# Kernel optimization log

Measured on AMD Instinct MI355X. Metric: run time of the kernel, lower is better.

## Reference

```python
import jax, jax.numpy as jnp
import numpy as np

D_HEAD = 128
WINDOW = 512
SCALE = D_HEAD ** -0.5

def setup_inputs() -> dict:
    key = jax.random.key(0)
    kq, kk, kv = jax.random.split(key, 3)
    shape = (4, 16, 2048, D_HEAD)  # [B, H, T, d_head]
    q = jax.random.normal(kq, shape, dtype=jnp.float32)
    k = jax.random.normal(kk, shape, dtype=jnp.float32)
    v = jax.random.normal(kv, shape, dtype=jnp.float32)
    return {"q": q, "k": k, "v": v}

def reference(q, k, v):
    # Sliding-window causal attention (BaseAttention._sliding_window_attention).
    T = q.shape[2]
    scores = jnp.einsum('bhqd,bhkd->bhqk', q, k) * SCALE  # [B,H,T,T]
    i = jnp.arange(T)
    causal = i[None, :] <= i[:, None]                      # j <= i
    in_window = (i[:, None] - i[None, :]) < WINDOW         # i - j < window
    mask = causal & in_window
    scores = jnp.where(mask, scores, -jnp.inf)
    attn = jax.nn.softmax(scores.astype(jnp.float32), axis=-1).astype(v.dtype)
    return jnp.einsum('bhqk,bhkd->bhqd', attn, v)
```

## Files before the change

kernel.cpp:

```cpp
#include <hip/hip_runtime.h>

#define T_SEQ   2048
#define DH      128
#define WINDOW  512
#define BM      128
#define BN      64
#define NT      32
#define TILE_US 16384
#define SCALE_LOG2E 0.12751744250f

typedef unsigned short ushort_t;
typedef __attribute__((ext_vector_type(8))) unsigned short ushort8;
typedef __attribute__((ext_vector_type(4))) unsigned short ushort4v;
typedef __attribute__((ext_vector_type(4))) float float4v;
typedef __attribute__((ext_vector_type(16))) float float16v;
typedef __attribute__((ext_vector_type(8))) __bf16 bf16x8;

union U8 { ushort8 us; bf16x8 bf; unsigned u[4]; };
union FU { float f; unsigned u; };

__device__ __forceinline__ unsigned short f2bf(float f) {
  FU x; x.f = f;
  unsigned r = x.u + 0x7FFFu + ((x.u >> 16) & 1u);
  return (unsigned short)(r >> 16);
}

__device__ __forceinline__ void async16(const ushort_t* g, ushort_t* l) {
  __builtin_amdgcn_global_load_lds(
      (const __attribute__((address_space(1))) unsigned int*)g,
      (__attribute__((address_space(3))) unsigned int*)l, 16, 0, 0);
}

__global__ __launch_bounds__(256)
void pack_kv(const float* __restrict__ kg, const float* __restrict__ vg,
             ushort_t* __restrict__ ws)
{
  __shared__ __align__(16) ushort_t sb[TILE_US];
  const int tile = blockIdx.x;
  const int tid  = threadIdx.x;
  const size_t src = (size_t)tile * (BN * DH);
  const float* kb = kg + src;
  const float* vb = vg + src;

#pragma unroll
  for (int rep = 0; rep < 4; ++rep) {
    const int b   = rep * 256 + tid;
    const int key = b >> 4;
    const int c8  = b & 15;
    const float* s = kb + key * DH + c8 * 8;
    float4v a = *(const float4v*)s;
    float4v c = *(const float4v*)(s + 4);
    U8 h;
    h.us[0]=f2bf(a[0]); h.us[1]=f2bf(a[1]); h.us[2]=f2bf(a[2]); h.us[3]=f2bf(a[3]);
    h.us[4]=f2bf(c[0]); h.us[5]=f2bf(c[1]); h.us[6]=f2bf(c[2]); h.us[7]=f2bf(c[3]);
    *(ushort8*)(sb + key * DH + ((c8 ^ (key & 7)) << 3)) = h.us;
  }

  {
    const int cb  = tid >> 3;
    const int rb0 = tid & 7;
#pragma unroll
    for (int it = 0; it < 2; ++it) {
      const int rb = rb0 + it * 8;
      const float* s = vb + (size_t)(rb * 4) * DH + cb * 4;
      float4v r0 = *(const float4v*)(s);
      float4v r1 = *(const float4v*)(s + DH);
      float4v r2 = *(const float4v*)(s + 2 * DH);
      float4v r3 = *(const float4v*)(s + 3 * DH);
      const int B    = (rb & 1) | ((rb >> 2) << 1);
      const int off4 = ((rb >> 1) & 1) << 2;
#pragma unroll
      for (int c = 0; c < 4; ++c) {
        const int d = cb * 4 + c;
        ushort4v h;
        h[0]=f2bf(r0[c]); h[1]=f2bf(r1[c]); h[2]=f2bf(r2[c]); h[3]=f2bf(r3[c]);
        *(ushort4v*)(sb + 8192 + d * BN + ((B ^ (d & 7)) << 3) + off4) = h;
      }
    }
  }
  __syncthreads();

  ushort_t* wt = ws + (size_t)tile * TILE_US;
#pragma unroll
  for (int rep = 0; rep < 8; ++rep) {
    const int off = (rep * 256 + tid) * 8;
    *(ushort8*)(wt + off) = *(const ushort8*)(sb + off);
  }
}

__global__ __launch_bounds__(256, 3)
void swa_fwd(const float* __restrict__ qg, const ushort_t* __restrict__ ws,
             float* __restrict__ og)
{
  __shared__ __align__(16) ushort_t lds[TILE_US];

  const int qt   = (gridDim.x - 1) - blockIdx.x;
  const int bh   = blockIdx.y;
  const int tid  = threadIdx.x;
  const int wv   = tid >> 6;
  const int lane = tid & 63;
  const int l32  = lane & 31;
  const int half = lane >> 5;
  const int l7   = l32 & 7;

  const size_t base = (size_t)bh * (T_SEQ * DH);
  const float* qb = qg + base;
  float*       ob = og + base;
  const ushort_t* wsb = ws + (size_t)bh * NT * TILE_US;

  const int i0w = qt * BM + wv * 32;
  const int iq  = i0w + l32;

  bf16x8 qf[8];
  {
    const float* qrow = qb + (size_t)iq * DH + half * 8;
#pragma unroll
    for (int ks = 0; ks < 8; ++ks) {
      float4v a = *(const float4v*)(qrow + ks * 16);
      float4v b = *(const float4v*)(qrow + ks * 16 + 4);
      U8 u;
      u.us[0]=f2bf(a[0]*SCALE_LOG2E); u.us[1]=f2bf(a[1]*SCALE_LOG2E);
      u.us[2]=f2bf(a[2]*SCALE_LOG2E); u.us[3]=f2bf(a[3]*SCALE_LOG2E);
      u.us[4]=f2bf(b[0]*SCALE_LOG2E); u.us[5]=f2bf(b[1]*SCALE_LOG2E);
      u.us[6]=f2bf(b[2]*SCALE_LOG2E); u.us[7]=f2bf(b[3]*SCALE_LOG2E);
      qf[ks] = u.bf;
    }
  }

  float16v O[4];
#pragma unroll
  for (int dc = 0; dc < 4; ++dc) O[dc] = (float16v)(0.0f);
  float m = -1e30f, l = 0.f;

  const int lo  = qt * BM - (WINDOW - 1);
  const int kt0 = (lo > 0) ? (lo >> 6) : 0;
  const int kt1 = 2 * qt + 1;

  for (int kt = kt0; kt <= kt1; ++kt) {
    {
      const ushort_t* wt = wsb + (size_t)kt * TILE_US;
#pragma unroll
      for (int rd = 0; rd < 8; ++rd) {
        const int off = (rd * 256 + tid) * 8;
        async16(wt + off, lds + off);
      }
    }
    __syncthreads();

    const int j0 = kt * BN;
    const bool active = (j0 <= i0w + 31) && (i0w - j0 - 63 < WINDOW);
    if (active) {
      float16v sv[2];
#pragma unroll
      for (int c = 0; c < 2; ++c) {
        float16v acc = (float16v)(0.0f);
        const ushort_t* krow = lds + (c * 32 + l32) * DH;
#pragma unroll
        for (int ks = 0; ks < 8; ++ks) {
          U8 a; a.us = *(const ushort8*)(krow + (((2 * ks + half) ^ l7) << 3));
          acc = __builtin_amdgcn_mfma_f32_32x32x16_bf16(a.bf, qf[ks], acc, 0, 0, 0);
        }
        sv[c] = acc;
      }

      const bool full = (j0 + 63 <= i0w) && ((i0w + 31) - j0 < WINDOW);
      if (!full) {
#pragma unroll
        for (int c = 0; c < 2; ++c) {
#pragma unroll
          for (int r = 0; r < 16; ++r) {
            const int j = j0 + c * 32 + (r & 3) + 8 * (r >> 2) + 4 * half;
            const bool ok = (j <= iq) && ((iq - j) < WINDOW);
            sv[c][r] = ok ? sv[c][r] : -1e30f;
          }
        }
      }

      float mt = sv[0][0];
#pragma unroll
      for (int r = 1; r < 16; ++r) mt = fmaxf(mt, sv[0][r]);
#pragma unroll
      for (int r = 0; r < 16; ++r) mt = fmaxf(mt, sv[1][r]);
      mt = fmaxf(mt, __shfl_xor(mt, 32));
      const float mn = fmaxf(m, mt);
      const float alpha = __builtin_amdgcn_exp2f(m - mn);
      m = mn;

      float ps = 0.f;
      unsigned pk[2][8];
#pragma unroll
      for (int c = 0; c < 2; ++c) {
#pragma unroll
        for (int rg = 0; rg < 8; ++rg) {
          FU p0, p1;
          p0.f = __builtin_amdgcn_exp2f(sv[c][2 * rg]     - m);
          p1.f = __builtin_amdgcn_exp2f(sv[c][2 * rg + 1] - m);
          p0.u &= 0xFFFF0000u; p1.u &= 0xFFFF0000u;
          ps += p0.f + p1.f;
          pk[c][rg] = (p0.u >> 16) | p1.u;
        }
      }
      l = l * alpha + ps;
#pragma unroll
      for (int dc = 0; dc < 4; ++dc)
#pragma unroll
        for (int r = 0; r < 16; ++r) O[dc][r] *= alpha;

#pragma unroll
      for (int s = 0; s < 4; ++s) {
        const int c = s >> 1, o = (s & 1) * 4;
        U8 b;
        b.u[0] = pk[c][o]; b.u[1] = pk[c][o + 1];
        b.u[2] = pk[c][o + 2]; b.u[3] = pk[c][o + 3];
        const int blk = ((2 * s + half) ^ l7) << 3;
#pragma unroll
        for (int dc = 0; dc < 4; ++dc) {
          U8 a; a.us = *(const ushort8*)(lds + 8192 + (dc * 32 + l32) * BN + blk);
          O[dc] = __builtin_amdgcn_mfma_f32_32x32x16_bf16(a.bf, b.bf, O[dc], 0, 0, 0);
        }
      }
    }
    __syncthreads();
  }

  l += __shfl_xor(l, 32);
  const float linv = 1.0f / l;
  float* orow = ob + (size_t)iq * DH;
#pragma unroll
  for (int dc = 0; dc < 4; ++dc) {
#pragma unroll
    for (int g = 0; g < 4; ++g) {
      float4v o4;
      o4[0] = O[dc][g * 4 + 0] * linv; o4[1] = O[dc][g * 4 + 1] * linv;
      o4[2] = O[dc][g * 4 + 2] * linv; o4[3] = O[dc][g * 4 + 3] * linv;
      *(float4v*)(orow + dc * 32 + g * 8 + half * 4) = o4;
    }
  }
}

extern "C" void kernel_launch(void* const* d_in, const int* in_sizes, int n_in,
                              void* d_out, int out_size, void* d_ws, size_t ws_size,
                              hipStream_t stream) {
  const float* q = (const float*)d_in[0];
  const float* k = (const float*)d_in[1];
  const float* v = (const float*)d_in[2];
  float* o = (float*)d_out;
  const int bh_count = in_sizes[0] / (T_SEQ * DH);
  ushort_t* ws = (ushort_t*)d_ws;

  pack_kv<<<dim3(bh_count * NT), 256, 0, stream>>>(k, v, ws);
  swa_fwd<<<dim3(T_SEQ / BM, bh_count), 256, 0, stream>>>(q, ws, o);
}
```

Measured before the change: 279.0 us.

## Pipeline K/V tile loads with a rotating three-slot LDS buffer

Splits each packed K/V tile into K and V halves and rotates them through three LDS slots. The next tile's V half and the tile after that's K half are prefetched asynchronously while the current QK^T and PV MFMAs run, with vmcnt waits and raw barriers replacing the load-then-sync pattern. The aim is to hide global-to-LDS latency behind compute. It also raises wave priority around the MFMA sections. In exchange, LDS use grows by half, which may lower occupancy at three blocks per CU, and the hand-counted waitcnt and barrier logic is fragile.

```diff
diff --git a/kernel.cpp b/kernel.cpp
--- a/kernel.cpp
+++ b/kernel.cpp
@@ -7,6 +7,7 @@
 #define BN      64
 #define NT      32
 #define TILE_US 16384
+#define HALF_US 8192
 #define SCALE_LOG2E 0.12751744250f
 
 typedef unsigned short ushort_t;
@@ -30,6 +31,19 @@
       (const __attribute__((address_space(1))) unsigned int*)g,
       (__attribute__((address_space(3))) unsigned int*)l, 16, 0, 0);
 }
+
+__device__ __forceinline__ void stage_half(const ushort_t* __restrict__ src,
+                                           ushort_t* __restrict__ dst,
+                                           const int tid) {
+#pragma unroll
+  for (int rd = 0; rd < 4; ++rd) {
+    const int off = (rd * 256 + tid) * 8;
+    async16(src + off, dst + off);
+  }
+}
+
+#define WAITV(N) asm volatile("s_waitcnt vmcnt(" #N ")" ::: "memory")
+#define MEMFENCE asm volatile("" ::: "memory")
 
 __global__ __launch_bounds__(256)
 void pack_kv(const float* __restrict__ kg, const float* __restrict__ vg,
@@ -92,7 +106,7 @@
 void swa_fwd(const float* __restrict__ qg, const ushort_t* __restrict__ ws,
              float* __restrict__ og)
 {
-  __shared__ __align__(16) ushort_t lds[TILE_US];
+  __shared__ __align__(16) ushort_t lds[3 * HALF_US];
 
   const int qt   = (gridDim.x - 1) - blockIdx.x;
   const int bh   = blockIdx.y;
@@ -110,6 +124,20 @@
 
   const int i0w = qt * BM + wv * 32;
   const int iq  = i0w + l32;
+
+  const int lo  = qt * BM - (WINDOW - 1);
+  const int kt0 = (lo > 0) ? (lo >> 6) : 0;
+  const int kt1 = 2 * qt + 1;
+
+  int sa = 0, sb = HALF_US, sc = 2 * HALF_US;
+
+  {
+    const ushort_t* wt0 = wsb + (size_t)kt0 * TILE_US;
+    stage_half(wt0,           lds + sa, tid);
+    stage_half(wt0 + HALF_US, lds + sb, tid);
+    if (kt0 < kt1)
+      stage_half(wt0 + TILE_US, lds + sc, tid);
+  }
 
   bf16x8 qf[8];
   {
@@ -132,29 +160,21 @@
   for (int dc = 0; dc < 4; ++dc) O[dc] = (float16v)(0.0f);
   float m = -1e30f, l = 0.f;
 
-  const int lo  = qt * BM - (WINDOW - 1);
-  const int kt0 = (lo > 0) ? (lo >> 6) : 0;
-  const int kt1 = 2 * qt + 1;
+  if (kt0 < kt1) { WAITV(8); } else { WAITV(4); }
+  __builtin_amdgcn_s_barrier();
+  MEMFENCE;
 
   for (int kt = kt0; kt <= kt1; ++kt) {
-    {
-      const ushort_t* wt = wsb + (size_t)kt * TILE_US;
-#pragma unroll
-      for (int rd = 0; rd < 8; ++rd) {
-        const int off = (rd * 256 + tid) * 8;
-        async16(wt + off, lds + off);
-      }
-    }
-    __syncthreads();
-
     const int j0 = kt * BN;
     const bool active = (j0 <= i0w + 31) && (i0w - j0 - 63 < WINDOW);
+
+    float16v sv[2];
     if (active) {
-      float16v sv[2];
+      __builtin_amdgcn_s_setprio(1);
 #pragma unroll
       for (int c = 0; c < 2; ++c) {
         float16v acc = (float16v)(0.0f);
-        const ushort_t* krow = lds + (c * 32 + l32) * DH;
+        const ushort_t* krow = lds + sa + (c * 32 + l32) * DH;
 #pragma unroll
         for (int ks = 0; ks < 8; ++ks) {
           U8 a; a.us = *(const ushort8*)(krow + (((2 * ks + half) ^ l7) << 3));
@@ -162,7 +182,16 @@
         }
         sv[c] = acc;
       }
-
+      __builtin_amdgcn_s_setprio(0);
+    }
+
+    MEMFENCE;
+    __builtin_amdgcn_s_barrier();
+    MEMFENCE;
+    if (kt < kt1)
+      stage_half(wsb + (size_t)(kt + 1) * TILE_US + HALF_US, lds + sa, tid);
+
+    if (active) {
       const bool full = (j0 + 63 <= i0w) && ((i0w + 31) - j0 < WINDOW);
       if (!full) {
 #pragma unroll
@@ -206,6 +235,11 @@
 #pragma unroll
         for (int r = 0; r < 16; ++r) O[dc][r] *= alpha;
 
+      if (kt < kt1) { WAITV(8); } else { WAITV(0); }
+      __builtin_amdgcn_s_barrier();
+      MEMFENCE;
+
+      __builtin_amdgcn_s_setprio(1);
 #pragma unroll
       for (int s = 0; s < 4; ++s) {
         const int c = s >> 1, o = (s & 1) * 4;
@@ -215,12 +249,32 @@
         const int blk = ((2 * s + half) ^ l7) << 3;
 #pragma unroll
         for (int dc = 0; dc < 4; ++dc) {
-          U8 a; a.us = *(const ushort8*)(lds + 8192 + (dc * 32 + l32) * BN + blk);
+          U8 a; a.us = *(const ushort8*)(lds + sb + (dc * 32 + l32) * BN + blk);
           O[dc] = __builtin_amdgcn_mfma_f32_32x32x16_bf16(a.bf, b.bf, O[dc], 0, 0, 0);
         }
       }
-    }
-    __syncthreads();
+      __builtin_amdgcn_s_setprio(0);
+    } else {
+      if (kt < kt1) { WAITV(8); } else { WAITV(0); }
+      __builtin_amdgcn_s_barrier();
+      MEMFENCE;
+    }
+
+    if (kt < kt1) {
+      MEMFENCE;
+      __builtin_amdgcn_s_barrier();
+      MEMFENCE;
+      if (kt + 2 <= kt1) {
+        stage_half(wsb + (size_t)(kt + 2) * TILE_US, lds + sb, tid);
+        WAITV(8);
+      } else {
+        WAITV(4);
+      }
+      __builtin_amdgcn_s_barrier();
+      MEMFENCE;
+    }
+
+    const int t = sc; sc = sb; sb = sa; sa = t;
   }
 
   l += __shfl_xor(l, 32);
```

New measurement: 308.0 us. 1.1x slower.
